# Optimization experiments

Hardware: AMD Instinct MI355X
Metric: run time of the kernel (lower is better)

## Reference

```python
import jax, jax.numpy as jnp
import numpy as np

MIN_VARIANCE = 0.1
W_MEAN = 1.0
W_DIST = 1.0
W_DISP = 1.0


def setup_inputs() -> dict:
    key = jax.random.key(0)
    k1, k2 = jax.random.split(key)
    cluster1 = jax.random.normal(k1, (8192, 128), dtype=jnp.float32)
    cluster2 = jax.random.normal(k2, (8192, 128), dtype=jnp.float32)
    return {"cluster1": cluster1, "cluster2": cluster2}


def _mean_loss(c1, c2):
    m1 = jnp.mean(c1, axis=0)
    m2 = jnp.mean(c2, axis=0)
    return jnp.mean((m1 - m2) ** 2)  # F.mse_loss default 'mean'


def _distance_loss(c1, c2):
    # min_j ||c1_i - c2_j||^2, fused via ||a||^2 - 2 a b^T + ||b||^2
    sq1 = jnp.sum(c1 * c1, axis=1)  # [N1]
    sq2 = jnp.sum(c2 * c2, axis=1)  # [N2]
    cross = c1 @ c2.T               # [N1, N2]
    d2 = sq1[:, None] - 2.0 * cross + sq2[None, :]
    return jnp.mean(jnp.min(d2, axis=1))


def _dispersion_loss(c, min_variance=MIN_VARIANCE):
    mean = jnp.mean(c, axis=0)
    variances = jnp.mean((c - mean) ** 2, axis=0)
    return jnp.mean(jax.nn.relu(min_variance - variances))


def reference(cluster1, cluster2):
    return (W_MEAN * _mean_loss(cluster1, cluster2)
            + W_DIST * _distance_loss(cluster1, cluster2)
            + W_DISP * _dispersion_loss(cluster1))
```

## Files before the change

kernel.cpp:

```cpp
#include <hip/hip_runtime.h>
#include <hip/hip_bf16.h>

#define N_ROWS 8192
#define DIMS   128

typedef __bf16 bf16x8 __attribute__((ext_vector_type(8)));
typedef float  f32x4  __attribute__((ext_vector_type(4)));

struct alignas(8) B4 { __hip_bfloat16 h0, h1, h2, h3; };

template <int CTRL>
__device__ __forceinline__ float fmin_dpp(float v) {
    int o = __builtin_amdgcn_update_dpp(0, __float_as_int(v), CTRL, 0xF, 0xF, true);
    return fminf(v, __int_as_float(o));
}

__global__ __launch_bounds__(256) void prep_k(const float* __restrict__ c1,
                                              const float* __restrict__ c2,
                                              __hip_bfloat16* __restrict__ c1b,
                                              __hip_bfloat16* __restrict__ c2b,
                                              float* __restrict__ sq1,
                                              float* __restrict__ sq2,
                                              float* __restrict__ part,
                                              int* __restrict__ cnt) {
    const int tid  = threadIdx.x;
    const int lane = tid & 63;
    const int wave = tid >> 6;
    const int half = lane >> 5;
    const int l32  = lane & 31;
    const int cl   = blockIdx.x >> 7;
    const int blk  = blockIdx.x & 127;

    if (blockIdx.x == 0 && tid == 0) *cnt = 0;

    const float* __restrict__ src    = cl ? c2 : c1;
    __hip_bfloat16* __restrict__ dst = cl ? c2b : c1b;
    float* __restrict__ sq           = cl ? sq2 : sq1;
    const float scale                = cl ? 1.0f : -2.0f;

    float4 cs = {0.f, 0.f, 0.f, 0.f};
    float4 cq = {0.f, 0.f, 0.f, 0.f};

    #pragma unroll 4
    for (int i = 0; i < 8; ++i) {
        const int row = blk * 64 + wave * 16 + i * 2 + half;
        float4 x = *reinterpret_cast<const float4*>(src + (size_t)row * DIMS + l32 * 4);
        B4 b4{__float2bfloat16(scale * x.x), __float2bfloat16(scale * x.y),
              __float2bfloat16(scale * x.z), __float2bfloat16(scale * x.w)};
        const int eoff = cl ? (l32 * 4) : ((l32 * 4) ^ ((row & 7) << 3));
        *reinterpret_cast<B4*>(dst + (size_t)row * DIMS + eoff) = b4;
        float s = x.x * x.x + x.y * x.y + x.z * x.z + x.w * x.w;
        #pragma unroll
        for (int m = 16; m; m >>= 1) s += __shfl_xor(s, m);
        if (l32 == 0) sq[row] = s;
        cs.x += x.x; cs.y += x.y; cs.z += x.z; cs.w += x.w;
        cq.x += x.x * x.x; cq.y += x.y * x.y; cq.z += x.z * x.z; cq.w += x.w * x.w;
    }

    cs.x += __shfl_xor(cs.x, 32); cs.y += __shfl_xor(cs.y, 32);
    cs.z += __shfl_xor(cs.z, 32); cs.w += __shfl_xor(cs.w, 32);
    cq.x += __shfl_xor(cq.x, 32); cq.y += __shfl_xor(cq.y, 32);
    cq.z += __shfl_xor(cq.z, 32); cq.w += __shfl_xor(cq.w, 32);

    __shared__ float4 lds4[4][32];
    lds4[wave][l32] = cs;
    __syncthreads();
    if (tid < 32) {
        float4 a = lds4[0][tid], b = lds4[1][tid], c = lds4[2][tid], d = lds4[3][tid];
        float4 t = {a.x + b.x + c.x + d.x, a.y + b.y + c.y + d.y,
                    a.z + b.z + c.z + d.z, a.w + b.w + c.w + d.w};
        const int base = cl ? 32768 : 0;
        part[base + (4 * tid + 0) * 128 + blk] = t.x;
        part[base + (4 * tid + 1) * 128 + blk] = t.y;
        part[base + (4 * tid + 2) * 128 + blk] = t.z;
        part[base + (4 * tid + 3) * 128 + blk] = t.w;
    }
    __syncthreads();
    lds4[wave][l32] = cq;
    __syncthreads();
    if (tid < 32 && cl == 0) {
        float4 a = lds4[0][tid], b = lds4[1][tid], c = lds4[2][tid], d = lds4[3][tid];
        float4 t = {a.x + b.x + c.x + d.x, a.y + b.y + c.y + d.y,
                    a.z + b.z + c.z + d.z, a.w + b.w + c.w + d.w};
        part[16384 + (4 * tid + 0) * 128 + blk] = t.x;
        part[16384 + (4 * tid + 1) * 128 + blk] = t.y;
        part[16384 + (4 * tid + 2) * 128 + blk] = t.z;
        part[16384 + (4 * tid + 3) * 128 + blk] = t.w;
    }
}

__global__ __attribute__((amdgpu_flat_work_group_size(512, 512),
                          amdgpu_waves_per_eu(2, 4)))
void dist_k(const __hip_bfloat16* __restrict__ c1bs,
            const __hip_bfloat16* __restrict__ c2b,
            const float* __restrict__ sq2,
            float* __restrict__ pmin) {
    __shared__ uint4 smem4[4096];
    char* smem = (char*)smem4;

    const int tid  = threadIdx.x;
    const int lane = tid & 63;
    const int wv   = tid >> 6;
    const int lo = lane & 15;
    const int hi = lane >> 4;
    const int rg = blockIdx.x >> 4;
    const int cg = blockIdx.x & 15;
    const int row0 = rg * 256;
    const int col0 = cg * 512 + wv * 64;

    {
        const char* gsrc = (const char*)c1bs + (size_t)row0 * 256;
        #pragma unroll
        for (int i = 0; i < 8; ++i) {
            const int off = i * 8192 + wv * 1024;
            __builtin_amdgcn_global_load_lds(
                (const __attribute__((address_space(1))) unsigned int*)
                    (const void*)(gsrc + off + lane * 16),
                (__attribute__((address_space(3))) unsigned int*)
                    (void*)(smem + off),
                16, 0, 0);
        }
    }

    uint4 b_u[4][4];
    float sq2t[4];
    #pragma unroll
    for (int ct = 0; ct < 4; ++ct) {
        const int J = col0 + ct * 16 + lo;
        sq2t[ct] = sq2[J];
        #pragma unroll
        for (int ks = 0; ks < 4; ++ks)
            b_u[ct][ks] = *reinterpret_cast<const uint4*>(
                c2b + (size_t)J * DIMS + ks * 32 + hi * 8);
    }
    #pragma unroll
    for (int ct = 0; ct < 4; ++ct)
        #pragma unroll
        for (int ks = 0; ks < 4; ++ks)
            asm volatile("" : "+v"(b_u[ct][ks].x), "+v"(b_u[ct][ks].y),
                              "+v"(b_u[ct][ks].z), "+v"(b_u[ct][ks].w));

    asm volatile("s_waitcnt vmcnt(0)" ::: "memory");
    __syncthreads();

    const int swz = (lo & 7) << 4;
    for (int rt = 0; rt < 16; ++rt) {
        bf16x8 a[4];
        #pragma unroll
        for (int ks = 0; ks < 4; ++ks) {
            const int boff = (rt * 16 + lo) * 256 + ((ks * 64 + hi * 16) ^ swz);
            a[ks] = *reinterpret_cast<const bf16x8*>(smem + boff);
        }

        float mrow[4] = {__builtin_inff(), __builtin_inff(),
                         __builtin_inff(), __builtin_inff()};

        #pragma unroll
        for (int ct = 0; ct < 4; ++ct) {
            f32x4 acc = {sq2t[ct], sq2t[ct], sq2t[ct], sq2t[ct]};
            #pragma unroll
            for (int ks = 0; ks < 4; ++ks)
                acc = __builtin_amdgcn_mfma_f32_16x16x32_bf16(
                    a[ks], __builtin_bit_cast(bf16x8, b_u[ct][ks]), acc, 0, 0, 0);
            #pragma unroll
            for (int r = 0; r < 4; ++r)
                mrow[r] = fminf(mrow[r], acc[r]);
        }

        #pragma unroll
        for (int r = 0; r < 4; ++r) {
            float v = mrow[r];
            v = fmin_dpp<0xB1>(v);
            v = fmin_dpp<0x4E>(v);
            v = fmin_dpp<0x141>(v);
            v = fmin_dpp<0x140>(v);
            mrow[r] = v;
        }
        if (lo == 0) {
            #pragma unroll
            for (int r = 0; r < 4; ++r) {
                const int row = row0 + rt * 16 + hi * 4 + r;
                pmin[(size_t)row * 128 + cg * 8 + wv] = mrow[r];
            }
        }
    }
}

__global__ __launch_bounds__(256) void tail_k(const float* __restrict__ pmin,
                                              const float* __restrict__ sq1,
                                              const float* __restrict__ part,
                                              float* __restrict__ rscratch,
                                              float* __restrict__ cscratch,
                                              int* __restrict__ cnt,
                                              float* __restrict__ out) {
    __shared__ float red[256];
    __shared__ int is_last;
    const int b   = blockIdx.x;
    const int tid = threadIdx.x;

    const int row = b * 256 + tid;
    const float4* p = reinterpret_cast<const float4*>(pmin + (size_t)row * 128);
    float4 m4 = p[0];
    #pragma unroll
    for (int i = 1; i < 32; ++i) {
        float4 v = p[i];
        m4.x = fminf(m4.x, v.x); m4.y = fminf(m4.y, v.y);
        m4.z = fminf(m4.z, v.z); m4.w = fminf(m4.w, v.w);
    }
    float m = fminf(fminf(m4.x, m4.y), fminf(m4.z, m4.w)) + sq1[row];

    red[tid] = m;
    __syncthreads();
    for (int off = 128; off; off >>= 1) {
        if (tid < off) red[tid] += red[tid + off];
        __syncthreads();
    }
    if (tid == 0) rscratch[b] = red[0];

    if (tid < 12) {
        const int j = b * 12 + tid;
        const float4* q = reinterpret_cast<const float4*>(part + j * 128);
        float4 a = {0.f, 0.f, 0.f, 0.f};
        #pragma unroll 8
        for (int k = 0; k < 32; ++k) {
            float4 v = q[k];
            a.x += v.x; a.y += v.y; a.z += v.z; a.w += v.w;
        }
        cscratch[j] = a.x + a.y + a.z + a.w;
    }

    __threadfence();
    __syncthreads();
    if (tid == 0) {
        int old = atomicAdd(cnt, 1);
        is_last = (old == 31) ? 1 : 0;
    }
    __syncthreads();
    if (!is_last) return;
    __threadfence();

    float s = (tid < 32) ? atomicAdd(&rscratch[tid], 0.0f) : 0.0f;

    float mm = 0.f;
    if (tid < DIMS) {
        float cs1 = atomicAdd(&cscratch[tid], 0.0f);
        float cq1 = atomicAdd(&cscratch[128 + tid], 0.0f);
        float cs2 = atomicAdd(&cscratch[256 + tid], 0.0f);
        const float inv_n = 1.0f / N_ROWS;
        float m1 = cs1 * inv_n;
        float m2 = cs2 * inv_n;
        float d  = m1 - m2;
        float var = cq1 * inv_n - m1 * m1;
        mm = d * d + fmaxf(0.1f - var, 0.0f);
    }

    __syncthreads();
    red[tid] = s * (1.0f / N_ROWS) + mm * (1.0f / DIMS);
    __syncthreads();
    for (int off = 128; off; off >>= 1) {
        if (tid < off) red[tid] += red[tid + off];
        __syncthreads();
    }
    if (tid == 0) out[0] = red[0];
}

extern "C" void kernel_launch(void* const* d_in, const int* in_sizes, int n_in,
                              void* d_out, int out_size, void* d_ws, size_t ws_size,
                              hipStream_t stream) {
    (void)in_sizes; (void)n_in; (void)out_size; (void)ws_size;
    const float* c1 = (const float*)d_in[0];
    const float* c2 = (const float*)d_in[1];

    char* ws = (char*)d_ws;
    __hip_bfloat16* c1b = (__hip_bfloat16*)ws;
    __hip_bfloat16* c2b = (__hip_bfloat16*)(ws + (1u << 21));
    float* sq1          = (float*)(ws + (1u << 22));
    float* sq2          = sq1 + N_ROWS;
    float* pmin         = sq2 + N_ROWS;
    float* part         = pmin + (size_t)N_ROWS * 128;
    float* rscratch     = part + 3 * 16384;
    float* cscratch     = rscratch + 32;
    int*   cnt          = (int*)(cscratch + 384);

    prep_k<<<256, 256, 0, stream>>>(c1, c2, c1b, c2b, sq1, sq2, part, cnt);
    dist_k<<<512, 512, 0, stream>>>(c1b, c2b, sq2, pmin);
    tail_k<<<32, 256, 0, stream>>>(pmin, sq1, part, rscratch, cscratch, cnt,
                                   (float*)d_out);
}
```

Baseline: 46.91 us.

## Retile distance GEMM into 128x128 LDS-staged blocks with 2x2 wave tiles

The distance kernel is restructured from 512-thread blocks that stream 256 rows of A from LDS against per-wave register-resident B columns into 4096 blocks of 256 threads, each staging a 128x128 tile of both A and B in LDS. Each wave computes a 64x64 output tile with a 4x4 accumulator grid, which gives register-level reuse of both operands. The prep kernel now swizzles c2's bf16 layout the same way as c1 to support the LDS reads. In exchange the grid is eight times larger, with more global-to-LDS traffic per output and more accumulator registers per wave.

```diff
diff --git a/kernel.cpp b/kernel.cpp
--- a/kernel.cpp
+++ b/kernel.cpp
@@ -47,7 +47,7 @@
         float4 x = *reinterpret_cast<const float4*>(src + (size_t)row * DIMS + l32 * 4);
         B4 b4{__float2bfloat16(scale * x.x), __float2bfloat16(scale * x.y),
               __float2bfloat16(scale * x.z), __float2bfloat16(scale * x.w)};
-        const int eoff = cl ? (l32 * 4) : ((l32 * 4) ^ ((row & 7) << 3));
+        const int eoff = (l32 * 4) ^ ((row & 7) << 3);
         *reinterpret_cast<B4*>(dst + (size_t)row * DIMS + eoff) = b4;
         float s = x.x * x.x + x.y * x.y + x.z * x.z + x.w * x.w;
         #pragma unroll
@@ -89,10 +89,9 @@
     }
 }
 
-__global__ __attribute__((amdgpu_flat_work_group_size(512, 512),
-                          amdgpu_waves_per_eu(2, 4)))
+__global__ __launch_bounds__(256)
 void dist_k(const __hip_bfloat16* __restrict__ c1bs,
-            const __hip_bfloat16* __restrict__ c2b,
+            const __hip_bfloat16* __restrict__ c2bs,
             const float* __restrict__ sq2,
             float* __restrict__ pmin) {
     __shared__ uint4 smem4[4096];
@@ -103,73 +102,78 @@
     const int wv   = tid >> 6;
     const int lo = lane & 15;
     const int hi = lane >> 4;
-    const int rg = blockIdx.x >> 4;
-    const int cg = blockIdx.x & 15;
-    const int row0 = rg * 256;
-    const int col0 = cg * 512 + wv * 64;
+    const int rg = blockIdx.x >> 6;
+    const int cb = blockIdx.x & 63;
+    const int row0 = rg * 128;
+    const int colb = cb * 128;
+    const int wr = wv >> 1;
+    const int wc = wv & 1;
 
     {
-        const char* gsrc = (const char*)c1bs + (size_t)row0 * 256;
+        const char* gA = (const char*)c1bs + (size_t)row0 * 256;
+        const char* gB = (const char*)c2bs + (size_t)colb * 256;
         #pragma unroll
         for (int i = 0; i < 8; ++i) {
-            const int off = i * 8192 + wv * 1024;
+            const int off = i * 4096 + wv * 1024;
             __builtin_amdgcn_global_load_lds(
                 (const __attribute__((address_space(1))) unsigned int*)
-                    (const void*)(gsrc + off + lane * 16),
+                    (const void*)(gA + off + lane * 16),
                 (__attribute__((address_space(3))) unsigned int*)
-                    (void*)(smem + off),
-                16, 0, 0);
-        }
-    }
-
-    uint4 b_u[4][4];
+                    (void*)(smem + off), 16, 0, 0);
+            __builtin_amdgcn_global_load_lds(
+                (const __attribute__((address_space(1))) unsigned int*)
+                    (const void*)(gB + off + lane * 16),
+                (__attribute__((address_space(3))) unsigned int*)
+                    (void*)(smem + 32768 + off), 16, 0, 0);
+        }
+    }
+
     float sq2t[4];
     #pragma unroll
-    for (int ct = 0; ct < 4; ++ct) {
-        const int J = col0 + ct * 16 + lo;
-        sq2t[ct] = sq2[J];
-        #pragma unroll
-        for (int ks = 0; ks < 4; ++ks)
-            b_u[ct][ks] = *reinterpret_cast<const uint4*>(
-                c2b + (size_t)J * DIMS + ks * 32 + hi * 8);
-    }
-    #pragma unroll
     for (int ct = 0; ct < 4; ++ct)
-        #pragma unroll
-        for (int ks = 0; ks < 4; ++ks)
-            asm volatile("" : "+v"(b_u[ct][ks].x), "+v"(b_u[ct][ks].y),
-                              "+v"(b_u[ct][ks].z), "+v"(b_u[ct][ks].w));
+        sq2t[ct] = sq2[colb + wc * 64 + ct * 16 + lo];
+
+    f32x4 acc[4][4];
+    #pragma unroll
+    for (int rt = 0; rt < 4; ++rt)
+        #pragma unroll
+        for (int ct = 0; ct < 4; ++ct)
+            acc[rt][ct] = f32x4{sq2t[ct], sq2t[ct], sq2t[ct], sq2t[ct]};
 
     asm volatile("s_waitcnt vmcnt(0)" ::: "memory");
     __syncthreads();
 
     const int swz = (lo & 7) << 4;
-    for (int rt = 0; rt < 16; ++rt) {
-        bf16x8 a[4];
-        #pragma unroll
-        for (int ks = 0; ks < 4; ++ks) {
-            const int boff = (rt * 16 + lo) * 256 + ((ks * 64 + hi * 16) ^ swz);
-            a[ks] = *reinterpret_cast<const bf16x8*>(smem + boff);
-        }
-
-        float mrow[4] = {__builtin_inff(), __builtin_inff(),
-                         __builtin_inff(), __builtin_inff()};
-
+    #pragma unroll
+    for (int ks = 0; ks < 4; ++ks) {
+        bf16x8 a[4], b[4];
+        #pragma unroll
+        for (int rt = 0; rt < 4; ++rt) {
+            const int row = wr * 64 + rt * 16 + lo;
+            a[rt] = *reinterpret_cast<const bf16x8*>(
+                smem + row * 256 + ((ks * 64 + hi * 16) ^ swz));
+        }
         #pragma unroll
         for (int ct = 0; ct < 4; ++ct) {
-            f32x4 acc = {sq2t[ct], sq2t[ct], sq2t[ct], sq2t[ct]};
+            const int col = wc * 64 + ct * 16 + lo;
+            b[ct] = *reinterpret_cast<const bf16x8*>(
+                smem + 32768 + col * 256 + ((ks * 64 + hi * 16) ^ swz));
+        }
+        #pragma unroll
+        for (int rt = 0; rt < 4; ++rt)
             #pragma unroll
-            for (int ks = 0; ks < 4; ++ks)
-                acc = __builtin_amdgcn_mfma_f32_16x16x32_bf16(
-                    a[ks], __builtin_bit_cast(bf16x8, b_u[ct][ks]), acc, 0, 0, 0);
-            #pragma unroll
-            for (int r = 0; r < 4; ++r)
-                mrow[r] = fminf(mrow[r], acc[r]);
-        }
-
+            for (int ct = 0; ct < 4; ++ct)
+                acc[rt][ct] = __builtin_amdgcn_mfma_f32_16x16x32_bf16(
+                    a[rt], b[ct], acc[rt][ct], 0, 0, 0);
+    }
+
+    #pragma unroll
+    for (int rt = 0; rt < 4; ++rt) {
+        float mrow[4];
         #pragma unroll
         for (int r = 0; r < 4; ++r) {
-            float v = mrow[r];
+            float v = fminf(fminf(acc[rt][0][r], acc[rt][1][r]),
+                            fminf(acc[rt][2][r], acc[rt][3][r]));
             v = fmin_dpp<0xB1>(v);
             v = fmin_dpp<0x4E>(v);
             v = fmin_dpp<0x141>(v);
@@ -179,8 +183,8 @@
         if (lo == 0) {
             #pragma unroll
             for (int r = 0; r < 4; ++r) {
-                const int row = row0 + rt * 16 + hi * 4 + r;
-                pmin[(size_t)row * 128 + cg * 8 + wv] = mrow[r];
+                const int row = row0 + wr * 64 + rt * 16 + hi * 4 + r;
+                pmin[(size_t)row * 128 + cb * 2 + wc] = mrow[r];
             }
         }
     }
@@ -283,7 +287,7 @@
     int*   cnt          = (int*)(cscratch + 384);
 
     prep_k<<<256, 256, 0, stream>>>(c1, c2, c1b, c2b, sq1, sq2, part, cnt);
-    dist_k<<<512, 512, 0, stream>>>(c1b, c2b, sq2, pmin);
+    dist_k<<<4096, 256, 0, stream>>>(c1b, c2b, sq2, pmin);
     tail_k<<<32, 256, 0, stream>>>(pmin, sq1, part, rscratch, cscratch, cnt,
                                    (float*)d_out);
 }
```

Measured after the change: 53.27 us. 1.14x slower.
